# Optimization experiments

Measured on AMD Instinct MI355X. Metric: run time of the kernel, lower is better.

Reference implementation:

```python
import jax, jax.numpy as jnp
import numpy as np

SELECTOR = jnp.array([29, 49, 79])
N_FINAL = 6
N_EM_ITERS = 10
LOG_2PI = float(np.log(2.0 * np.pi))


def _logdet2(c):
    # log determinant of trailing 2x2 matrices
    return jnp.log(c[..., 0, 0] * c[..., 1, 1] - c[..., 0, 1] * c[..., 1, 0])


def _inv2(c):
    # analytic inverse of trailing 2x2 matrices
    det = c[..., 0, 0] * c[..., 1, 1] - c[..., 0, 1] * c[..., 1, 0]
    inv = jnp.stack([
        jnp.stack([c[..., 1, 1], -c[..., 0, 1]], axis=-1),
        jnp.stack([-c[..., 1, 0], c[..., 0, 0]], axis=-1),
    ], axis=-2)
    return inv / det[..., None, None]


def _initial_state(probas, trajectories):
    B, M = probas.shape
    tsel = trajectories[:, :, SELECTOR, :]                       # [B,M,3,2]
    dots = jnp.einsum('bmtd,bntd->btmn', tsel, tsel)             # [B,3,M,M]
    d1 = jnp.einsum('bmtd,bmtd->btm', tsel, tsel)                # [B,3,M]
    R = jnp.sqrt(d1[:, :, :, None] + d1[:, :, None, :] - 2.0 * dots)
    thr = jnp.quantile(R[:, -1].reshape(B, -1), 0.15, axis=-1)[:, None, None, None]
    adj = (R <= thr).astype(probas.dtype).prod(axis=1)           # [B,M,M]
    worked = jnp.ones((B, M), dtype=probas.dtype)
    bidx = jnp.arange(B)
    idxs = []
    for _ in range(N_FINAL):
        score = (adj * probas[:, None, :]).sum(axis=2) * worked  # [B,M]
        amax = jnp.argmax(score, axis=-1)                        # [B]
        worked = worked * (1.0 - adj[bidx, amax])
        idxs.append(amax)
    return jnp.stack(idxs, axis=1)                               # [B,6]


def _coefficients(cov6, trajectories, traj6, probas6):
    cov6_sel = cov6[:, :, SELECTOR]                              # [B,6,3,2,2]
    prec = _inv2(cov6_sel)                                       # [B,6,3,2,2]
    diff = traj6[:, :, SELECTOR][:, :, None] - trajectories[:, :, SELECTOR][:, None]  # [B,6,M,3,2]
    qform = jnp.einsum('bnmti,bntij,bnmtj->bnmt', diff, prec, diff)
    logdet = _logdet2(cov6_sel)[:, :, None, :]                   # [B,6,1,3]
    pM = jnp.exp((-LOG_2PI - 0.5 * logdet - 0.5 * qform).sum(axis=-1)) + 1e-8  # [B,6,M]
    num = pM * probas6[:, :, None]
    return num / (num.sum(axis=1, keepdims=True) + 1e-8)


def _forward(non_normalized_probas, trajectories, covariance_matrices):
    B = trajectories.shape[0]
    probas = jax.nn.softmax(non_normalized_probas, axis=-1)
    idx = jax.lax.stop_gradient(_initial_state(probas, trajectories))  # [B,6]
    b = jnp.arange(B)[:, None]
    traj6 = trajectories[b, idx]                                 # [B,6,T,2]
    probas6 = jax.nn.softmax(jnp.take_along_axis(non_normalized_probas, idx, axis=1), axis=-1)
    cov6 = covariance_matrices[b, idx]                           # [B,6,T,2,2]
    for _ in range(N_EM_ITERS):
        pM = jax.lax.stop_gradient(_coefficients(cov6, trajectories, traj6, probas6))
        P = probas[:, None, :] * pM                              # [B,6,M]
        probas6 = P.sum(axis=-1)                                 # [B,6]
        traj6 = jnp.einsum('bnm,bmtd->bntd', P, trajectories) / probas6[:, :, None, None]
        diff = traj6[:, :, None] - trajectories[:, None]         # [B,6,M,T,2]
        cov6 = (jnp.einsum('bnm,bmtij->bntij', P, covariance_matrices)
                + jnp.einsum('bnm,bnmti,bnmtj->bntij', P, diff, diff)) / probas6[:, :, None, None, None]
    return probas6, traj6, cov6


def setup_inputs() -> dict:
    key = jax.random.key(0)
    k1, k2, k3 = jax.random.split(key, 3)
    B, M, T = 256, 48, 80
    logits = jax.random.normal(k1, (B, M), dtype=jnp.float32)
    trajectories = jax.random.normal(k2, (B, M, T, 2), dtype=jnp.float32)
    A = 0.3 * jax.random.normal(k3, (B, M, T, 2, 2), dtype=jnp.float32)
    cov = A @ jnp.swapaxes(A, -1, -2) + 0.5 * jnp.eye(2, dtype=jnp.float32)
    return {'non_normalized_probas': logits, 'trajectories': trajectories,
            'covariance_matrices': cov}


def reference(non_normalized_probas, trajectories, covariance_matrices):
    return _forward(non_normalized_probas, trajectories, covariance_matrices)
```

## Files before the change

### kernel.cpp

```cpp
#include <hip/hip_runtime.h>
#include <math.h>

#define BATCH 256
#define M 48
#define T 80
#define NF 6
#define EMIT 10
#define MM (M*M)
#define KPL (MM/64)
#define NBIN 256
#define CAP 192
#define LOG2PI 1.8378770664093453f

typedef unsigned int u32;
typedef unsigned long long u64;

__global__ __launch_bounds__(64, 1)
void em_kernel(const float* __restrict__ g_logits,
               const float* __restrict__ g_traj,
               const float* __restrict__ g_cov,
               float* __restrict__ g_out)
{
    const int b = blockIdx.x;
    const int lane = threadIdx.x;
    const int SEL[3] = {29, 49, 79};

    __shared__ __align__(16) float s_txy[M*T*2];
    __shared__ __align__(16) float s_cv4[M*T*4];
    __shared__ float s_adj[MM];
    __shared__ float s_logits[M];
    __shared__ float s_probas[M];
    __shared__ float s_tsel[M*6];
    __shared__ float s_d1[M*3];
    __shared__ __align__(16) float s_csel[M*3*4];
    __shared__ __align__(16) float s_Pm[M*8];
    __shared__ float s_t6sel[NF*6];
    __shared__ float s_probas6[NF];
    __shared__ float s_prec[NF*3*3];
    __shared__ float s_ld[NF*3];
    __shared__ int   s_idx[NF];
    __shared__ u32   s_hist[NBIN];
    __shared__ u32   s_cand[CAP];
    __shared__ u32   s_cnt;
    __shared__ float s_v[2];

    const float* traj_b = g_traj + (size_t)b*(M*T*2);
    const float* cov_b  = g_cov  + (size_t)b*(M*T*4);

    float myLogit = -1e30f;
    if (lane < M) myLogit = g_logits[b*M + lane];
    float selx[3], sely[3], cc0[3], cc1[3], cc2[3];
    #pragma unroll
    for (int r = 0; r < 3; ++r) {
        int i = lane + r*64;
        if (i < M*3) {
            int m = i/3, tt = i - (i/3)*3;
            float2 xy = ((const float2*)traj_b)[m*T + SEL[tt]];
            float4 cv = ((const float4*)cov_b)[m*T + SEL[tt]];
            selx[r]=xy.x; sely[r]=xy.y; cc0[r]=cv.x; cc1[r]=cv.y; cc2[r]=cv.w;
        }
    }
    if (lane < M) s_logits[lane] = myLogit;
    #pragma unroll
    for (int r = 0; r < 3; ++r) {
        int i = lane + r*64;
        if (i < M*3) {
            int m = i/3, tt = i - (i/3)*3;
            s_tsel[m*6+tt*2+0] = selx[r];
            s_tsel[m*6+tt*2+1] = sely[r];
            s_d1[i] = selx[r]*selx[r] + sely[r]*sely[r];
            s_csel[i*4+0]=cc0[r]; s_csel[i*4+1]=cc1[r]; s_csel[i*4+2]=cc2[r]; s_csel[i*4+3]=0.f;
        }
    }

    __builtin_amdgcn_sched_barrier(0);
    {
        const char* gt = (const char*)traj_b + lane*16;
        #pragma unroll
        for (int k = 0; k < 30; ++k)
            __builtin_amdgcn_global_load_lds(
                (const __attribute__((address_space(1))) u32*)(gt + k*1024),
                (__attribute__((address_space(3))) u32*)((char*)s_txy + k*1024), 16, 0, 0);
    }
    __builtin_amdgcn_sched_barrier(0);

    float mx = myLogit;
    #pragma unroll
    for (int off = 32; off; off >>= 1) mx = fmaxf(mx, __shfl_xor(mx, off));
    float pe = (lane < M) ? expf(myLogit - mx) : 0.f;
    float psum = pe;
    #pragma unroll
    for (int off = 32; off; off >>= 1) psum += __shfl_xor(psum, off);
    const float proba = pe / psum;
    if (lane < M) s_probas[lane] = proba;

    float key[KPL];
    #pragma unroll
    for (int c = 0; c < KPL; ++c) {
        int e = lane + c*64;
        int m = e/M, n = e - (e/M)*M;
        float dot = s_tsel[m*6+4]*s_tsel[n*6+4] + s_tsel[m*6+5]*s_tsel[n*6+5];
        float v = s_d1[m*3+2] + s_d1[n*3+2] - 2.0f*dot;
        key[c] = sqrtf(fmaxf(v, 0.0f));
    }
    float kmax = 0.f;
    #pragma unroll
    for (int c = 0; c < KPL; ++c) kmax = fmaxf(kmax, key[c]);
    #pragma unroll
    for (int off = 32; off; off >>= 1) kmax = fmaxf(kmax, __shfl_xor(kmax, off));
    const float scale = 256.0f / kmax;

    s_hist[lane]=0; s_hist[lane+64]=0; s_hist[lane+128]=0; s_hist[lane+192]=0;
    #pragma unroll
    for (int c = 0; c < KPL; ++c) {
        int bin = (int)(key[c]*scale); bin = bin > 255 ? 255 : bin;
        atomicAdd(&s_hist[bin], 1u);
    }
    uint4 hv = ((const uint4*)s_hist)[lane];
    u32 s4 = hv.x + hv.y + hv.z + hv.w;
    u32 cum = s4;
    #pragma unroll
    for (int off = 1; off < 64; off <<= 1) {
        u32 u = __shfl_up(cum, off);
        if (lane >= off) cum += u;
    }

    #pragma unroll 1
    for (int ri = 0; ri < 2; ++ri) {
        const u32 target = 345u + (u32)ri;
        u64 bmask = __ballot(cum > target);
        int g = __builtin_ctzll(bmask);
        int binIdx = 0; u32 binStart = 0;
        if (lane == g) {
            u32 exc = cum - s4;
            int bi2 = lane*4;
            if (exc + hv.x > target)      { binIdx = bi2;   binStart = exc; }
            else { exc += hv.x;
                if (exc + hv.y > target)  { binIdx = bi2+1; binStart = exc; }
                else { exc += hv.y;
                    if (exc + hv.z > target) { binIdx = bi2+2; binStart = exc; }
                    else { exc += hv.z;       binIdx = bi2+3; binStart = exc; } } }
        }
        binIdx   = __shfl(binIdx, g);
        binStart = (u32)__shfl((int)binStart, g);
        if (lane == 0) s_cnt = 0;
        #pragma unroll
        for (int c = 0; c < KPL; ++c) {
            int bin = (int)(key[c]*scale); bin = bin > 255 ? 255 : bin;
            if (bin == binIdx) {
                u32 p = atomicAdd(&s_cnt, 1u);
                if (p < CAP) s_cand[p] = __float_as_uint(key[c]);
            }
        }
        u32 cnt = s_cnt; if (cnt > CAP) cnt = CAP;
        u32 own0=0xFFFFFFFFu, own1=0xFFFFFFFFu, own2=0xFFFFFFFFu;
        if ((u32)lane      < cnt) own0 = s_cand[lane];
        if ((u32)lane+64u  < cnt) own1 = s_cand[lane+64];
        if ((u32)lane+128u < cnt) own2 = s_cand[lane+128];
        u32 cl0=0,ce0=0, cl1=0,ce1=0, cl2=0,ce2=0;
        for (u32 i = 0; i < cnt; ++i) {
            u32 v = s_cand[i];
            cl0 += (v < own0); ce0 += (v == own0);
            cl1 += (v < own1); ce1 += (v == own1);
            cl2 += (v < own2); ce2 += (v == own2);
        }
        if ((u32)lane      < cnt && binStart+cl0 <= target && target < binStart+cl0+ce0) s_v[ri] = __uint_as_float(own0);
        if ((u32)lane+64u  < cnt && binStart+cl1 <= target && target < binStart+cl1+ce1) s_v[ri] = __uint_as_float(own1);
        if ((u32)lane+128u < cnt && binStart+cl2 <= target && target < binStart+cl2+ce2) s_v[ri] = __uint_as_float(own2);
    }
    const float qi = 0.15f * 2303.0f;
    const float fr = qi - floorf(qi);
    const float thr = s_v[0]*(1.0f - fr) + s_v[1]*fr;

    __builtin_amdgcn_sched_barrier(0);
    {
        const char* gc = (const char*)cov_b + lane*16;
        #pragma unroll
        for (int k = 0; k < 30; ++k)
            __builtin_amdgcn_global_load_lds(
                (const __attribute__((address_space(1))) u32*)(gc + k*1024),
                (__attribute__((address_space(3))) u32*)((char*)s_cv4 + k*1024), 16, 0, 0);
    }
    __builtin_amdgcn_sched_barrier(0);

    #pragma unroll
    for (int c = 0; c < KPL; ++c) {
        int e = lane + c*64;
        int m = e/M, n = e - (e/M)*M;
        float d0 = s_tsel[m*6+0]*s_tsel[n*6+0] + s_tsel[m*6+1]*s_tsel[n*6+1];
        float r0 = sqrtf(fmaxf(s_d1[m*3+0] + s_d1[n*3+0] - 2.0f*d0, 0.0f));
        float d1v = s_tsel[m*6+2]*s_tsel[n*6+2] + s_tsel[m*6+3]*s_tsel[n*6+3];
        float r1 = sqrtf(fmaxf(s_d1[m*3+1] + s_d1[n*3+1] - 2.0f*d1v, 0.0f));
        bool a = (key[c] <= thr) && (r0 <= thr) && (r1 <= thr);
        s_adj[e] = a ? 1.0f : 0.0f;
    }

    __builtin_amdgcn_sched_barrier(0);
    {
        const char* gc = (const char*)cov_b + lane*16;
        #pragma unroll
        for (int k = 30; k < 60; ++k)
            __builtin_amdgcn_global_load_lds(
                (const __attribute__((address_space(1))) u32*)(gc + k*1024),
                (__attribute__((address_space(3))) u32*)((char*)s_cv4 + k*1024), 16, 0, 0);
    }
    __builtin_amdgcn_sched_barrier(0);

    const int m = (lane < M) ? lane : (M-1);
    {
        float base = 0.f;
        #pragma unroll
        for (int n = 0; n < M; ++n) base += s_adj[n*M+m] * s_probas[n];
        float worked = 1.f;
        #pragma unroll 1
        for (int k = 0; k < NF; ++k) {
            float sc = (lane < M) ? base*worked : -1.f;
            int bi = lane;
            #pragma unroll
            for (int off = 32; off; off >>= 1) {
                float so = __shfl_down(sc, off);
                int io = __shfl_down(bi, off);
                if (so > sc || (so == sc && io < bi)) { sc = so; bi = io; }
            }
            int amax = __shfl(bi, 0);
            if (lane == 0) s_idx[k] = amax;
            worked *= (1.f - s_adj[amax*M+m]);
        }
    }

    if (lane < NF) {
        float mx6 = -1e30f;
        for (int j = 0; j < NF; ++j) mx6 = fmaxf(mx6, s_logits[s_idx[j]]);
        float sum6 = 0.f;
        for (int j = 0; j < NF; ++j) sum6 += expf(s_logits[s_idx[j]] - mx6);
        s_probas6[lane] = expf(s_logits[s_idx[lane]] - mx6) / sum6;
    }
    if (lane < NF*3) {
        int n = lane/3, tt = lane - (lane/3)*3;
        int m0 = s_idx[n];
        s_t6sel[n*6+tt*2+0] = s_tsel[m0*6+tt*2+0];
        s_t6sel[n*6+tt*2+1] = s_tsel[m0*6+tt*2+1];
        float c00 = s_csel[(m0*3+tt)*4+0];
        float c01 = s_csel[(m0*3+tt)*4+1];
        float c11 = s_csel[(m0*3+tt)*4+2];
        float det = c00*c11 - c01*c01;
        s_prec[lane*3+0] =  c11/det;
        s_prec[lane*3+1] = -c01/det;
        s_prec[lane*3+2] =  c00/det;
        s_ld[lane] = logf(det);
    }

    float tm0=s_tsel[m*6+0], tm1=s_tsel[m*6+1], tm2=s_tsel[m*6+2],
          tm3=s_tsel[m*6+3], tm4=s_tsel[m*6+4], tm5=s_tsel[m*6+5];
    const int item  = lane/3;
    const int chunk = lane - item*3;
    const int mn    = item/3;
    const int mtt   = item - (item/3)*3;

    #pragma unroll 1
    for (int it = 0; it < EMIT; ++it) {
        float num[NF]; float den = 1e-8f;
        #pragma unroll
        for (int n = 0; n < NF; ++n) {
            float lsum = s_ld[n*3+0] + s_ld[n*3+1] + s_ld[n*3+2];
            float dx0 = s_t6sel[n*6+0]-tm0, dy0 = s_t6sel[n*6+1]-tm1;
            float dx1 = s_t6sel[n*6+2]-tm2, dy1 = s_t6sel[n*6+3]-tm3;
            float dx2 = s_t6sel[n*6+4]-tm4, dy2 = s_t6sel[n*6+5]-tm5;
            float q = s_prec[(n*3+0)*3+0]*dx0*dx0 + 2.f*s_prec[(n*3+0)*3+1]*dx0*dy0 + s_prec[(n*3+0)*3+2]*dy0*dy0
                    + s_prec[(n*3+1)*3+0]*dx1*dx1 + 2.f*s_prec[(n*3+1)*3+1]*dx1*dy1 + s_prec[(n*3+1)*3+2]*dy1*dy1
                    + s_prec[(n*3+2)*3+0]*dx2*dx2 + 2.f*s_prec[(n*3+2)*3+1]*dx2*dy2 + s_prec[(n*3+2)*3+2]*dy2*dy2;
            num[n] = (expf(-3.f*LOG2PI - 0.5f*lsum - 0.5f*q) + 1e-8f) * s_probas6[n];
            den += num[n];
        }
        float f = proba / den;
        if (lane < M) {
            *(float4*)&s_Pm[m*8]   = make_float4(num[0]*f, num[1]*f, num[2]*f, num[3]*f);
            *(float2*)&s_Pm[m*8+4] = make_float2(num[4]*f, num[5]*f);
        }
        if (it == EMIT-1) break;

        if (lane < 54) {
            float SP=0,S1x=0,S1y=0,Sxx=0,Sxy=0,Syy=0,Cs0=0,Cs1=0,Cs2=0;
            int mbase = chunk*16;
            #pragma unroll 4
            for (int k = 0; k < 16; ++k) {
                int mm = mbase + k;
                float p = s_Pm[mm*8+mn];
                float x = s_tsel[mm*6+mtt*2+0];
                float y = s_tsel[mm*6+mtt*2+1];
                float4 c4 = *(const float4*)&s_csel[(mm*3+mtt)*4];
                SP += p; S1x += p*x; S1y += p*y;
                Sxx += p*x*x; Sxy += p*x*y; Syy += p*y*y;
                Cs0 += p*c4.x; Cs1 += p*c4.y; Cs2 += p*c4.z;
            }
            #define CMB(v) { float a1_=__shfl_down(v,1), a2_=__shfl_down(v,2); v += a1_ + a2_; }
            CMB(SP) CMB(S1x) CMB(S1y) CMB(Sxx) CMB(Sxy) CMB(Syy) CMB(Cs0) CMB(Cs1) CMB(Cs2)
            if (chunk == 0) {
                float p6 = SP;
                if (mtt == 0) s_probas6[mn] = SP;
                float tx = S1x/p6, ty = S1y/p6;
                float c00 = (Cs0 + (Sxx - S1x*tx)) / p6;
                float c01 = (Cs1 + (Sxy - S1x*ty)) / p6;
                float c11 = (Cs2 + (Syy - S1y*ty)) / p6;
                float det = c00*c11 - c01*c01;
                s_prec[item*3+0] =  c11/det;
                s_prec[item*3+1] = -c01/det;
                s_prec[item*3+2] =  c00/det;
                s_ld[item] = logf(det);
                s_t6sel[mn*6+mtt*2+0] = tx;
                s_t6sel[mn*6+mtt*2+1] = ty;
            }
        }
    }

    __builtin_amdgcn_s_waitcnt(0x0F70);
    float*  out_p = g_out;
    float2* out_t = (float2*)(g_out + BATCH*NF);
    float4* out_c = (float4*)(g_out + BATCH*NF + BATCH*NF*T*2);
    #pragma unroll 1
    for (int t = lane; t < T; t += 64) {
        float SP[NF]={0,0,0,0,0,0}, S1x[NF]={0,0,0,0,0,0}, S1y[NF]={0,0,0,0,0,0};
        float Sxx[NF]={0,0,0,0,0,0}, Sxy[NF]={0,0,0,0,0,0}, Syy[NF]={0,0,0,0,0,0};
        float C00[NF]={0,0,0,0,0,0}, C01[NF]={0,0,0,0,0,0}, C11[NF]={0,0,0,0,0,0};
        #pragma unroll 2
        for (int mm = 0; mm < M; ++mm) {
            float2 xy = ((const float2*)s_txy)[mm*T + t];
            float4 c4 = ((const float4*)s_cv4)[mm*T + t];
            float4 Pa = *(const float4*)&s_Pm[mm*8];
            float2 Pb = *(const float2*)&s_Pm[mm*8+4];
            float xx = xy.x*xy.x, xyv = xy.x*xy.y, yy = xy.y*xy.y;
            #define UPD(p, n) { SP[n]+=(p); S1x[n]+=(p)*xy.x; S1y[n]+=(p)*xy.y; \
                Sxx[n]+=(p)*xx; Sxy[n]+=(p)*xyv; Syy[n]+=(p)*yy; \
                C00[n]+=(p)*c4.x; C01[n]+=(p)*c4.y; C11[n]+=(p)*c4.w; }
            UPD(Pa.x,0) UPD(Pa.y,1) UPD(Pa.z,2) UPD(Pa.w,3) UPD(Pb.x,4) UPD(Pb.y,5)
            #undef UPD
        }
        #pragma unroll
        for (int n = 0; n < NF; ++n) {
            float p6 = SP[n];
            float tx = S1x[n]/p6, ty = S1y[n]/p6;
            float c00 = (C00[n] + (Sxx[n] - S1x[n]*tx)) / p6;
            float c01 = (C01[n] + (Sxy[n] - S1x[n]*ty)) / p6;
            float c11 = (C11[n] + (Syy[n] - S1y[n]*ty)) / p6;
            size_t o = (size_t)(b*NF + n)*T + t;
            out_t[o] = make_float2(tx, ty);
            out_c[o] = make_float4(c00, c01, c01, c11);
        }
    }
    if (lane < NF) {
        float sp = 0.f;
        for (int mm = 0; mm < M; ++mm) sp += s_Pm[mm*8+lane];
        out_p[b*NF + lane] = sp;
    }
}

extern "C" void kernel_launch(void* const* d_in, const int* in_sizes, int n_in,
                              void* d_out, int out_size, void* d_ws, size_t ws_size,
                              hipStream_t stream) {
    const float* logits = (const float*)d_in[0];
    const float* traj   = (const float*)d_in[1];
    const float* cov    = (const float*)d_in[2];
    float* out = (float*)d_out;
    em_kernel<<<dim3(BATCH), dim3(64), 0, stream>>>(logits, traj, cov, out);
}
```

Baseline: 128.1 us.

## Use four waves per block with redundant EM and radix-select quantile

```diff
diff --git a/kernel.cpp b/kernel.cpp
--- a/kernel.cpp
+++ b/kernel.cpp
@@ -8,21 +8,21 @@
 #define EMIT 10
 #define MM (M*M)
 #define KPL (MM/64)
-#define NBIN 256
-#define CAP 192
 #define LOG2PI 1.8378770664093453f
 
 typedef unsigned int u32;
 typedef unsigned long long u64;
 
-__global__ __launch_bounds__(64, 1)
+__global__ __launch_bounds__(256, 1)
 void em_kernel(const float* __restrict__ g_logits,
                const float* __restrict__ g_traj,
                const float* __restrict__ g_cov,
                float* __restrict__ g_out)
 {
     const int b = blockIdx.x;
-    const int lane = threadIdx.x;
+    const int tid = threadIdx.x;
+    const int lane = tid & 63;
+    const int wv = tid >> 6;
     const int SEL[3] = {29, 49, 79};
 
     __shared__ __align__(16) float s_txy[M*T*2];
@@ -33,16 +33,13 @@
     __shared__ float s_tsel[M*6];
     __shared__ float s_d1[M*3];
     __shared__ __align__(16) float s_csel[M*3*4];
-    __shared__ __align__(16) float s_Pm[M*8];
-    __shared__ float s_t6sel[NF*6];
-    __shared__ float s_probas6[NF];
-    __shared__ float s_prec[NF*3*3];
-    __shared__ float s_ld[NF*3];
-    __shared__ int   s_idx[NF];
-    __shared__ u32   s_hist[NBIN];
-    __shared__ u32   s_cand[CAP];
-    __shared__ u32   s_cnt;
-    __shared__ float s_v[2];
+    __shared__ __align__(16) float s_Pm[4][M*8];
+    __shared__ float s_t6sel[4][NF*6];
+    __shared__ float s_probas6[4][NF];
+    __shared__ float s_prec[4][NF*3*3];
+    __shared__ float s_ld[4][NF*3];
+    __shared__ int   s_idx[4][8];
+    __shared__ __align__(16) u32 s_hist[4][256];
 
     const float* traj_b = g_traj + (size_t)b*(M*T*2);
     const float* cov_b  = g_cov  + (size_t)b*(M*T*4);
@@ -60,6 +57,26 @@
             selx[r]=xy.x; sely[r]=xy.y; cc0[r]=cv.x; cc1[r]=cv.y; cc2[r]=cv.w;
         }
     }
+
+    __builtin_amdgcn_sched_barrier(0);
+    {
+        const char* gt = (const char*)traj_b + lane*16;
+        char* lt = (char*)s_txy;
+        #pragma unroll 2
+        for (int k = wv; k < 30; k += 4)
+            __builtin_amdgcn_global_load_lds(
+                (const __attribute__((address_space(1))) u32*)(gt + k*1024),
+                (__attribute__((address_space(3))) u32*)(lt + k*1024), 16, 0, 0);
+        const char* gc = (const char*)cov_b + lane*16;
+        char* lc = (char*)s_cv4;
+        #pragma unroll 2
+        for (int k = wv; k < 60; k += 4)
+            __builtin_amdgcn_global_load_lds(
+                (const __attribute__((address_space(1))) u32*)(gc + k*1024),
+                (__attribute__((address_space(3))) u32*)(lc + k*1024), 16, 0, 0);
+    }
+    __builtin_amdgcn_sched_barrier(0);
+
     if (lane < M) s_logits[lane] = myLogit;
     #pragma unroll
     for (int r = 0; r < 3; ++r) {
@@ -73,115 +90,88 @@
         }
     }
 
-    __builtin_amdgcn_sched_barrier(0);
-    {
-        const char* gt = (const char*)traj_b + lane*16;
-        #pragma unroll
-        for (int k = 0; k < 30; ++k)
-            __builtin_amdgcn_global_load_lds(
-                (const __attribute__((address_space(1))) u32*)(gt + k*1024),
-                (__attribute__((address_space(3))) u32*)((char*)s_txy + k*1024), 16, 0, 0);
-    }
-    __builtin_amdgcn_sched_barrier(0);
-
     float mx = myLogit;
     #pragma unroll
     for (int off = 32; off; off >>= 1) mx = fmaxf(mx, __shfl_xor(mx, off));
-    float pe = (lane < M) ? expf(myLogit - mx) : 0.f;
+    float pe = (lane < M) ? __expf(myLogit - mx) : 0.f;
     float psum = pe;
     #pragma unroll
     for (int off = 32; off; off >>= 1) psum += __shfl_xor(psum, off);
     const float proba = pe / psum;
     if (lane < M) s_probas[lane] = proba;
 
-    float key[KPL];
+    u32 key[KPL];
     #pragma unroll
     for (int c = 0; c < KPL; ++c) {
         int e = lane + c*64;
         int m = e/M, n = e - (e/M)*M;
         float dot = s_tsel[m*6+4]*s_tsel[n*6+4] + s_tsel[m*6+5]*s_tsel[n*6+5];
         float v = s_d1[m*3+2] + s_d1[n*3+2] - 2.0f*dot;
-        key[c] = sqrtf(fmaxf(v, 0.0f));
-    }
-    float kmax = 0.f;
-    #pragma unroll
-    for (int c = 0; c < KPL; ++c) kmax = fmaxf(kmax, key[c]);
-    #pragma unroll
-    for (int off = 32; off; off >>= 1) kmax = fmaxf(kmax, __shfl_xor(kmax, off));
-    const float scale = 256.0f / kmax;
-
-    s_hist[lane]=0; s_hist[lane+64]=0; s_hist[lane+128]=0; s_hist[lane+192]=0;
-    #pragma unroll
-    for (int c = 0; c < KPL; ++c) {
-        int bin = (int)(key[c]*scale); bin = bin > 255 ? 255 : bin;
-        atomicAdd(&s_hist[bin], 1u);
-    }
-    uint4 hv = ((const uint4*)s_hist)[lane];
-    u32 s4 = hv.x + hv.y + hv.z + hv.w;
-    u32 cum = s4;
-    #pragma unroll
-    for (int off = 1; off < 64; off <<= 1) {
-        u32 u = __shfl_up(cum, off);
-        if (lane >= off) cum += u;
-    }
-
+        key[c] = __float_as_uint(sqrtf(fmaxf(v, 0.0f)));
+    }
+
+    u32* hist = &s_hist[wv][0];
+    int target = 345;
+    u32 prefix = 0u, pmask = 0u;
     #pragma unroll 1
-    for (int ri = 0; ri < 2; ++ri) {
-        const u32 target = 345u + (u32)ri;
-        u64 bmask = __ballot(cum > target);
+    for (int shift = 24; shift >= 0; shift -= 8) {
+        ((uint4*)hist)[lane] = make_uint4(0,0,0,0);
+        #pragma unroll
+        for (int c = 0; c < KPL; ++c) {
+            if ((key[c] & pmask) == prefix)
+                atomicAdd(&hist[(key[c] >> shift) & 255u], 1u);
+        }
+        uint4 hv = ((const uint4*)hist)[lane];
+        u32 s4 = hv.x + hv.y + hv.z + hv.w;
+        u32 cum = s4;
+        #pragma unroll
+        for (int off = 1; off < 64; off <<= 1) {
+            u32 u = __shfl_up(cum, off);
+            if (lane >= off) cum += u;
+        }
+        u64 bmask = __ballot(cum > (u32)target);
         int g = __builtin_ctzll(bmask);
-        int binIdx = 0; u32 binStart = 0;
+        int dig = 0; u32 binstart = 0;
         if (lane == g) {
             u32 exc = cum - s4;
             int bi2 = lane*4;
-            if (exc + hv.x > target)      { binIdx = bi2;   binStart = exc; }
+            if (exc + hv.x > (u32)target)      { dig = bi2;   binstart = exc; }
             else { exc += hv.x;
-                if (exc + hv.y > target)  { binIdx = bi2+1; binStart = exc; }
+                if (exc + hv.y > (u32)target)  { dig = bi2+1; binstart = exc; }
                 else { exc += hv.y;
-                    if (exc + hv.z > target) { binIdx = bi2+2; binStart = exc; }
-                    else { exc += hv.z;       binIdx = bi2+3; binStart = exc; } } }
-        }
-        binIdx   = __shfl(binIdx, g);
-        binStart = (u32)__shfl((int)binStart, g);
-        if (lane == 0) s_cnt = 0;
+                    if (exc + hv.z > (u32)target) { dig = bi2+2; binstart = exc; }
+                    else { exc += hv.z;            dig = bi2+3; binstart = exc; } } }
+        }
+        dig = __shfl(dig, g);
+        binstart = (u32)__shfl((int)binstart, g);
+        target -= (int)binstart;
+        prefix |= ((u32)dig) << shift;
+        pmask  |= (255u << shift);
+    }
+    const u32 k1 = prefix;
+    const float v1f = __uint_as_float(k1);
+
+    float v2f;
+    {
+        u32 cnt = 0, mng = 0xFFFFFFFFu;
         #pragma unroll
         for (int c = 0; c < KPL; ++c) {
-            int bin = (int)(key[c]*scale); bin = bin > 255 ? 255 : bin;
-            if (bin == binIdx) {
-                u32 p = atomicAdd(&s_cnt, 1u);
-                if (p < CAP) s_cand[p] = __float_as_uint(key[c]);
-            }
-        }
-        u32 cnt = s_cnt; if (cnt > CAP) cnt = CAP;
-        u32 own0=0xFFFFFFFFu, own1=0xFFFFFFFFu, own2=0xFFFFFFFFu;
-        if ((u32)lane      < cnt) own0 = s_cand[lane];
-        if ((u32)lane+64u  < cnt) own1 = s_cand[lane+64];
-        if ((u32)lane+128u < cnt) own2 = s_cand[lane+128];
-        u32 cl0=0,ce0=0, cl1=0,ce1=0, cl2=0,ce2=0;
-        for (u32 i = 0; i < cnt; ++i) {
-            u32 v = s_cand[i];
-            cl0 += (v < own0); ce0 += (v == own0);
-            cl1 += (v < own1); ce1 += (v == own1);
-            cl2 += (v < own2); ce2 += (v == own2);
-        }
-        if ((u32)lane      < cnt && binStart+cl0 <= target && target < binStart+cl0+ce0) s_v[ri] = __uint_as_float(own0);
-        if ((u32)lane+64u  < cnt && binStart+cl1 <= target && target < binStart+cl1+ce1) s_v[ri] = __uint_as_float(own1);
-        if ((u32)lane+128u < cnt && binStart+cl2 <= target && target < binStart+cl2+ce2) s_v[ri] = __uint_as_float(own2);
+            if (key[c] <= k1) cnt++;
+            else mng = (key[c] < mng) ? key[c] : mng;
+        }
+        #pragma unroll
+        for (int off = 32; off > 0; off >>= 1) {
+            cnt += __shfl_down(cnt, off);
+            u32 mo = (u32)__shfl_down((int)mng, off);
+            mng = (mo < mng) ? mo : mng;
+        }
+        u32 ct = (u32)__shfl((int)cnt, 0);
+        u32 mt = (u32)__shfl((int)mng, 0);
+        v2f = (ct >= 347u) ? v1f : __uint_as_float(mt);
     }
     const float qi = 0.15f * 2303.0f;
     const float fr = qi - floorf(qi);
-    const float thr = s_v[0]*(1.0f - fr) + s_v[1]*fr;
-
-    __builtin_amdgcn_sched_barrier(0);
-    {
-        const char* gc = (const char*)cov_b + lane*16;
-        #pragma unroll
-        for (int k = 0; k < 30; ++k)
-            __builtin_amdgcn_global_load_lds(
-                (const __attribute__((address_space(1))) u32*)(gc + k*1024),
-                (__attribute__((address_space(3))) u32*)((char*)s_cv4 + k*1024), 16, 0, 0);
-    }
-    __builtin_amdgcn_sched_barrier(0);
+    const float thr = v1f*(1.0f - fr) + v2f*fr;
 
     #pragma unroll
     for (int c = 0; c < KPL; ++c) {
@@ -191,20 +181,9 @@
         float r0 = sqrtf(fmaxf(s_d1[m*3+0] + s_d1[n*3+0] - 2.0f*d0, 0.0f));
         float d1v = s_tsel[m*6+2]*s_tsel[n*6+2] + s_tsel[m*6+3]*s_tsel[n*6+3];
         float r1 = sqrtf(fmaxf(s_d1[m*3+1] + s_d1[n*3+1] - 2.0f*d1v, 0.0f));
-        bool a = (key[c] <= thr) && (r0 <= thr) && (r1 <= thr);
+        bool a = (__uint_as_float(key[c]) <= thr) && (r0 <= thr) && (r1 <= thr);
         s_adj[e] = a ? 1.0f : 0.0f;
     }
-
-    __builtin_amdgcn_sched_barrier(0);
-    {
-        const char* gc = (const char*)cov_b + lane*16;
-        #pragma unroll
-        for (int k = 30; k < 60; ++k)
-            __builtin_amdgcn_global_load_lds(
-                (const __attribute__((address_space(1))) u32*)(gc + k*1024),
-                (__attribute__((address_space(3))) u32*)((char*)s_cv4 + k*1024), 16, 0, 0);
-    }
-    __builtin_amdgcn_sched_barrier(0);
 
     const int m = (lane < M) ? lane : (M-1);
     {
@@ -223,31 +202,33 @@
                 if (so > sc || (so == sc && io < bi)) { sc = so; bi = io; }
             }
             int amax = __shfl(bi, 0);
-            if (lane == 0) s_idx[k] = amax;
+            if (lane == 0) s_idx[wv][k] = amax;
             worked *= (1.f - s_adj[amax*M+m]);
         }
     }
 
     if (lane < NF) {
         float mx6 = -1e30f;
-        for (int j = 0; j < NF; ++j) mx6 = fmaxf(mx6, s_logits[s_idx[j]]);
+        #pragma unroll
+        for (int j = 0; j < NF; ++j) mx6 = fmaxf(mx6, s_logits[s_idx[wv][j]]);
         float sum6 = 0.f;
-        for (int j = 0; j < NF; ++j) sum6 += expf(s_logits[s_idx[j]] - mx6);
-        s_probas6[lane] = expf(s_logits[s_idx[lane]] - mx6) / sum6;
+        #pragma unroll
+        for (int j = 0; j < NF; ++j) sum6 += __expf(s_logits[s_idx[wv][j]] - mx6);
+        s_probas6[wv][lane] = __expf(s_logits[s_idx[wv][lane]] - mx6) / sum6;
     }
     if (lane < NF*3) {
         int n = lane/3, tt = lane - (lane/3)*3;
-        int m0 = s_idx[n];
-        s_t6sel[n*6+tt*2+0] = s_tsel[m0*6+tt*2+0];
-        s_t6sel[n*6+tt*2+1] = s_tsel[m0*6+tt*2+1];
+        int m0 = s_idx[wv][n];
+        s_t6sel[wv][n*6+tt*2+0] = s_tsel[m0*6+tt*2+0];
+        s_t6sel[wv][n*6+tt*2+1] = s_tsel[m0*6+tt*2+1];
         float c00 = s_csel[(m0*3+tt)*4+0];
         float c01 = s_csel[(m0*3+tt)*4+1];
         float c11 = s_csel[(m0*3+tt)*4+2];
         float det = c00*c11 - c01*c01;
-        s_prec[lane*3+0] =  c11/det;
-        s_prec[lane*3+1] = -c01/det;
-        s_prec[lane*3+2] =  c00/det;
-        s_ld[lane] = logf(det);
+        s_prec[wv][lane*3+0] =  c11/det;
+        s_prec[wv][lane*3+1] = -c01/det;
+        s_prec[wv][lane*3+2] =  c00/det;
+        s_ld[wv][lane] = __logf(det);
     }
 
     float tm0=s_tsel[m*6+0], tm1=s_tsel[m*6+1], tm2=s_tsel[m*6+2],
@@ -256,26 +237,27 @@
     const int chunk = lane - item*3;
     const int mn    = item/3;
     const int mtt   = item - (item/3)*3;
+    const int mslot = (mn < 3) ? mn : mn + 1;
 
     #pragma unroll 1
     for (int it = 0; it < EMIT; ++it) {
         float num[NF]; float den = 1e-8f;
         #pragma unroll
         for (int n = 0; n < NF; ++n) {
-            float lsum = s_ld[n*3+0] + s_ld[n*3+1] + s_ld[n*3+2];
-            float dx0 = s_t6sel[n*6+0]-tm0, dy0 = s_t6sel[n*6+1]-tm1;
-            float dx1 = s_t6sel[n*6+2]-tm2, dy1 = s_t6sel[n*6+3]-tm3;
-            float dx2 = s_t6sel[n*6+4]-tm4, dy2 = s_t6sel[n*6+5]-tm5;
-            float q = s_prec[(n*3+0)*3+0]*dx0*dx0 + 2.f*s_prec[(n*3+0)*3+1]*dx0*dy0 + s_prec[(n*3+0)*3+2]*dy0*dy0
-                    + s_prec[(n*3+1)*3+0]*dx1*dx1 + 2.f*s_prec[(n*3+1)*3+1]*dx1*dy1 + s_prec[(n*3+1)*3+2]*dy1*dy1
-                    + s_prec[(n*3+2)*3+0]*dx2*dx2 + 2.f*s_prec[(n*3+2)*3+1]*dx2*dy2 + s_prec[(n*3+2)*3+2]*dy2*dy2;
-            num[n] = (expf(-3.f*LOG2PI - 0.5f*lsum - 0.5f*q) + 1e-8f) * s_probas6[n];
+            float lsum = s_ld[wv][n*3+0] + s_ld[wv][n*3+1] + s_ld[wv][n*3+2];
+            float dx0 = s_t6sel[wv][n*6+0]-tm0, dy0 = s_t6sel[wv][n*6+1]-tm1;
+            float dx1 = s_t6sel[wv][n*6+2]-tm2, dy1 = s_t6sel[wv][n*6+3]-tm3;
+            float dx2 = s_t6sel[wv][n*6+4]-tm4, dy2 = s_t6sel[wv][n*6+5]-tm5;
+            float q = s_prec[wv][(n*3+0)*3+0]*dx0*dx0 + 2.f*s_prec[wv][(n*3+0)*3+1]*dx0*dy0 + s_prec[wv][(n*3+0)*3+2]*dy0*dy0
+                    + s_prec[wv][(n*3+1)*3+0]*dx1*dx1 + 2.f*s_prec[wv][(n*3+1)*3+1]*dx1*dy1 + s_prec[wv][(n*3+1)*3+2]*dy1*dy1
+                    + s_prec[wv][(n*3+2)*3+0]*dx2*dx2 + 2.f*s_prec[wv][(n*3+2)*3+1]*dx2*dy2 + s_prec[wv][(n*3+2)*3+2]*dy2*dy2;
+            num[n] = (__expf(-3.f*LOG2PI - 0.5f*lsum - 0.5f*q) + 1e-8f) * s_probas6[wv][n];
             den += num[n];
         }
         float f = proba / den;
         if (lane < M) {
-            *(float4*)&s_Pm[m*8]   = make_float4(num[0]*f, num[1]*f, num[2]*f, num[3]*f);
-            *(float2*)&s_Pm[m*8+4] = make_float2(num[4]*f, num[5]*f);
+            *(float4*)&s_Pm[wv][m*8]   = make_float4(num[0]*f, num[1]*f, num[2]*f, 0.f);
+            *(float4*)&s_Pm[wv][m*8+4] = make_float4(num[3]*f, num[4]*f, num[5]*f, 0.f);
         }
         if (it == EMIT-1) break;
 
@@ -285,7 +267,7 @@
             #pragma unroll 4
             for (int k = 0; k < 16; ++k) {
                 int mm = mbase + k;
-                float p = s_Pm[mm*8+mn];
+                float p = s_Pm[wv][mm*8 + mslot];
                 float x = s_tsel[mm*6+mtt*2+0];
                 float y = s_tsel[mm*6+mtt*2+1];
                 float4 c4 = *(const float4*)&s_csel[(mm*3+mtt)*4];
@@ -297,59 +279,64 @@
             CMB(SP) CMB(S1x) CMB(S1y) CMB(Sxx) CMB(Sxy) CMB(Syy) CMB(Cs0) CMB(Cs1) CMB(Cs2)
             if (chunk == 0) {
                 float p6 = SP;
-                if (mtt == 0) s_probas6[mn] = SP;
+                if (mtt == 0) s_probas6[wv][mn] = SP;
                 float tx = S1x/p6, ty = S1y/p6;
                 float c00 = (Cs0 + (Sxx - S1x*tx)) / p6;
                 float c01 = (Cs1 + (Sxy - S1x*ty)) / p6;
                 float c11 = (Cs2 + (Syy - S1y*ty)) / p6;
                 float det = c00*c11 - c01*c01;
-                s_prec[item*3+0] =  c11/det;
-                s_prec[item*3+1] = -c01/det;
-                s_prec[item*3+2] =  c00/det;
-                s_ld[item] = logf(det);
-                s_t6sel[mn*6+mtt*2+0] = tx;
-                s_t6sel[mn*6+mtt*2+1] = ty;
+                s_prec[wv][item*3+0] =  c11/det;
+                s_prec[wv][item*3+1] = -c01/det;
+                s_prec[wv][item*3+2] =  c00/det;
+                s_ld[wv][item] = __logf(det);
+                s_t6sel[wv][mn*6+mtt*2+0] = tx;
+                s_t6sel[wv][mn*6+mtt*2+1] = ty;
             }
         }
     }
 
-    __builtin_amdgcn_s_waitcnt(0x0F70);
+    __syncthreads();
+
     float*  out_p = g_out;
     float2* out_t = (float2*)(g_out + BATCH*NF);
     float4* out_c = (float4*)(g_out + BATCH*NF + BATCH*NF*T*2);
-    #pragma unroll 1
-    for (int t = lane; t < T; t += 64) {
-        float SP[NF]={0,0,0,0,0,0}, S1x[NF]={0,0,0,0,0,0}, S1y[NF]={0,0,0,0,0,0};
-        float Sxx[NF]={0,0,0,0,0,0}, Sxy[NF]={0,0,0,0,0,0}, Syy[NF]={0,0,0,0,0,0};
-        float C00[NF]={0,0,0,0,0,0}, C01[NF]={0,0,0,0,0,0}, C11[NF]={0,0,0,0,0,0};
-        #pragma unroll 2
+    if (lane < 40) {
+        int it2 = wv*40 + lane;
+        int t = it2 >> 1, half = it2 & 1;
+        float SP[3]={0,0,0}, S1x[3]={0,0,0}, S1y[3]={0,0,0};
+        float Sxx[3]={0,0,0}, Sxy[3]={0,0,0}, Syy[3]={0,0,0};
+        float C00[3]={0,0,0}, C01[3]={0,0,0}, C11[3]={0,0,0};
+        #pragma unroll 4
         for (int mm = 0; mm < M; ++mm) {
             float2 xy = ((const float2*)s_txy)[mm*T + t];
             float4 c4 = ((const float4*)s_cv4)[mm*T + t];
-            float4 Pa = *(const float4*)&s_Pm[mm*8];
-            float2 Pb = *(const float2*)&s_Pm[mm*8+4];
+            float4 pq = *(const float4*)&s_Pm[wv][mm*8 + half*4];
+            float p[3] = {pq.x, pq.y, pq.z};
             float xx = xy.x*xy.x, xyv = xy.x*xy.y, yy = xy.y*xy.y;
-            #define UPD(p, n) { SP[n]+=(p); S1x[n]+=(p)*xy.x; S1y[n]+=(p)*xy.y; \
-                Sxx[n]+=(p)*xx; Sxy[n]+=(p)*xyv; Syy[n]+=(p)*yy; \
-                C00[n]+=(p)*c4.x; C01[n]+=(p)*c4.y; C11[n]+=(p)*c4.w; }
-            UPD(Pa.x,0) UPD(Pa.y,1) UPD(Pa.z,2) UPD(Pa.w,3) UPD(Pb.x,4) UPD(Pb.y,5)
-            #undef UPD
-        }
-        #pragma unroll
-        for (int n = 0; n < NF; ++n) {
-            float p6 = SP[n];
-            float tx = S1x[n]/p6, ty = S1y[n]/p6;
-            float c00 = (C00[n] + (Sxx[n] - S1x[n]*tx)) / p6;
-            float c01 = (C01[n] + (Sxy[n] - S1x[n]*ty)) / p6;
-            float c11 = (C11[n] + (Syy[n] - S1y[n]*ty)) / p6;
+            #pragma unroll
+            for (int j = 0; j < 3; ++j) {
+                SP[j]+=p[j]; S1x[j]+=p[j]*xy.x; S1y[j]+=p[j]*xy.y;
+                Sxx[j]+=p[j]*xx; Sxy[j]+=p[j]*xyv; Syy[j]+=p[j]*yy;
+                C00[j]+=p[j]*c4.x; C01[j]+=p[j]*c4.y; C11[j]+=p[j]*c4.w;
+            }
+        }
+        #pragma unroll
+        for (int j = 0; j < 3; ++j) {
+            int n = half*3 + j;
+            float p6 = SP[j];
+            float tx = S1x[j]/p6, ty = S1y[j]/p6;
+            float c00 = (C00[j] + (Sxx[j] - S1x[j]*tx)) / p6;
+            float c01 = (C01[j] + (Sxy[j] - S1x[j]*ty)) / p6;
+            float c11 = (C11[j] + (Syy[j] - S1y[j]*ty)) / p6;
             size_t o = (size_t)(b*NF + n)*T + t;
             out_t[o] = make_float2(tx, ty);
             out_c[o] = make_float4(c00, c01, c01, c11);
         }
     }
-    if (lane < NF) {
+    if (wv == 0 && lane < NF) {
+        int slot = (lane < 3) ? lane : lane + 1;
         float sp = 0.f;
-        for (int mm = 0; mm < M; ++mm) sp += s_Pm[mm*8+lane];
+        for (int mm = 0; mm < M; ++mm) sp += s_Pm[0][mm*8 + slot];
         out_p[b*NF + lane] = sp;
     }
 }
@@ -361,5 +348,5 @@
     const float* traj   = (const float*)d_in[1];
     const float* cov    = (const float*)d_in[2];
     float* out = (float*)d_out;
-    em_kernel<<<dim3(BATCH), dim3(64), 0, stream>>>(logits, traj, cov, out);
+    em_kernel<<<dim3(BATCH), dim3(256), 0, stream>>>(logits, traj, cov, out);
 }
```

Result: faster. 122.3 us (-4.5%).
